# Performance work log

Measured on AMD Instinct MI355X. Metric: run time of the kernel, lower is better.

Reference implementation:

```python
import jax, jax.numpy as jnp
import numpy as np

B, D, NB, BS = 32, 2048, 16, 512  # batch, dim_input=dim_output, n_blocks, block_size; NB*BS*BS == D*D


def setup_inputs() -> dict:
    key = jax.random.key(0)
    k1, k2, k3, k4, k5 = jax.random.split(key, 5)
    x = jax.random.normal(k1, (B, D), dtype=jnp.float32)
    gate_w = jax.random.normal(k2, (D, NB), dtype=jnp.float32) / np.sqrt(D)
    gate_b = jax.random.normal(k3, (NB,), dtype=jnp.float32) * 0.02
    weight = jax.random.normal(k4, (D, D), dtype=jnp.float32) / np.sqrt(D)  # kaiming-uniform-like scale
    bias = jax.random.normal(k5, (D,), dtype=jnp.float32) * (1.0 / np.sqrt(D))
    return {"x": x, "gate_w": gate_w, "gate_b": gate_b, "weight": weight, "bias": bias}


def reference(x, gate_w, gate_b, weight, bias):
    b = x.shape[0]
    k_drop = NB // 2
    # gate network: Linear -> Sigmoid
    g = jax.nn.sigmoid(x @ gate_w + gate_b)  # (b, NB)
    # zero out the k smallest gates per sample (topk largest=False, scatter 0)
    _, drop_idx = jax.lax.top_k(-g, k_drop)  # indices of smallest gates
    rows = jnp.arange(b)[:, None]
    g = g.at[rows, drop_idx].set(0.0)
    # broadcast gates over block-diagonal chunks of weight
    w0 = weight.reshape(NB, BS, BS)
    gw = (g[:, :, None, None] * w0).reshape(b, D, D)  # (b, dim_output, dim_input)
    # batched matvec + bias
    return jnp.einsum('bij,bj->bi', gw, x) + bias
```

## Files before the change

### kernel.cpp

```cpp
#include <hip/hip_runtime.h>
#include <hip/hip_bf16.h>


#define D_DIM 2048
#define B_DIM 32
#define NB_DIM 16
#define NWAVE 8
#define KCHUNK (D_DIM / NWAVE)
#define PM_PAD 20

typedef __attribute__((ext_vector_type(4))) float f32x4;
typedef __attribute__((ext_vector_type(8))) float f32x8;
typedef __attribute__((ext_vector_type(8))) __bf16 bf16x8;

static __device__ __forceinline__ __bf16 f2bf(float f) {
    unsigned u = __builtin_bit_cast(unsigned, f);
    u += 0x7fffu + ((u >> 16) & 1u);
    unsigned short h = (unsigned short)(u >> 16);
    return __builtin_bit_cast(__bf16, h);
}

static __device__ __forceinline__ bf16x8 load_cvt8(const float* p) {
    const f32x8 v = *(const f32x8*)p;
    bf16x8 r;
#pragma unroll
    for (int i = 0; i < 8; ++i) r[i] = f2bf(v[i]);
    return r;
}

__global__ __launch_bounds__(256) void prep_kernel(
    const float* __restrict__ X,
    const float* __restrict__ GW,
    const float* __restrict__ GB,
    float* __restrict__ gates,
    __bf16* __restrict__ Xbf)
{
    __shared__ float red[NB_DIM][256];
    __shared__ float sg[NB_DIM];
    const int b = blockIdx.x;
    const int t = threadIdx.x;

    {
        const int idx = b * D_DIM + t * 8;
        *(bf16x8*)(Xbf + idx) = load_cvt8(X + idx);
    }

    float acc[NB_DIM];
#pragma unroll
    for (int n = 0; n < NB_DIM; ++n) acc[n] = 0.f;

#pragma unroll
    for (int i = 0; i < D_DIM / 256; ++i) {
        const int c = t + i * 256;
        const float xv = X[b * D_DIM + c];
        const float* gw = GW + c * NB_DIM;
#pragma unroll
        for (int n = 0; n < NB_DIM; ++n) acc[n] += xv * gw[n];
    }
#pragma unroll
    for (int n = 0; n < NB_DIM; ++n) red[n][t] = acc[n];
    __syncthreads();
    for (int s = 128; s > 0; s >>= 1) {
        if (t < s) {
#pragma unroll
            for (int n = 0; n < NB_DIM; ++n) red[n][t] += red[n][t + s];
        }
        __syncthreads();
    }
    if (t < NB_DIM) {
        const float v = red[t][0] + GB[t];
        sg[t] = 1.f / (1.f + __expf(-v));
    }
    __syncthreads();
    if (t < NB_DIM) {
        const float g = sg[t];
        int rank = 0;
#pragma unroll
        for (int m = 0; m < NB_DIM; ++m) {
            const float gm = sg[m];
            if (gm < g || (gm == g && m < t)) rank++;
        }
        gates[b * NB_DIM + t] = (rank >= NB_DIM / 2) ? g : 0.f;
    }
}

__global__ __launch_bounds__(512) void main_fused(
    const float* __restrict__ W,
    const __bf16* __restrict__ Xbf,
    const float* __restrict__ gates,
    const float* __restrict__ bias,
    float* __restrict__ out)
{
    __shared__ float pm[NWAVE * B_DIM * PM_PAD];

    const int rt   = blockIdx.x;
    const int wave = threadIdx.x >> 6;
    const int lane = threadIdx.x & 63;
    const int l15  = lane & 15;
    const int q    = lane >> 4;

    const int r0 = rt * 16;
    const int k0 = wave * KCHUNK;

    const float*  arow = W   + (size_t)(r0 + l15) * D_DIM + k0 + q * 8;
    const __bf16* b0p  = Xbf + (size_t)(l15)      * D_DIM + k0 + q * 8;
    const __bf16* b1p  = Xbf + (size_t)(l15 + 16) * D_DIM + k0 + q * 8;

    f32x4 acc0 = {0.f, 0.f, 0.f, 0.f};
    f32x4 acc1 = {0.f, 0.f, 0.f, 0.f};

#pragma unroll
    for (int kk = 0; kk < KCHUNK / 32; ++kk) {
        const bf16x8 av  = load_cvt8(arow + kk * 32);
        const bf16x8 bv0 = *(const bf16x8*)(b0p + kk * 32);
        const bf16x8 bv1 = *(const bf16x8*)(b1p + kk * 32);
        acc0 = __builtin_amdgcn_mfma_f32_16x16x32_bf16(av, bv0, acc0, 0, 0, 0);
        acc1 = __builtin_amdgcn_mfma_f32_16x16x32_bf16(av, bv1, acc1, 0, 0, 0);
    }

    float* base = pm + wave * (B_DIM * PM_PAD);
    *(f32x4*)(base + l15 * PM_PAD + q * 4)        = acc0;
    *(f32x4*)(base + (l15 + 16) * PM_PAD + q * 4) = acc1;
    __syncthreads();

    const int t   = threadIdx.x;
    const int lb  = t >> 4;
    const int row = t & 15;
    float s = 0.f;
#pragma unroll
    for (int w = 0; w < NWAVE; ++w)
        s += pm[w * (B_DIM * PM_PAD) + lb * PM_PAD + row];

    const float g  = gates[lb * NB_DIM + (r0 >> 7)];
    const float bi = bias[r0 + row];
    out[(size_t)lb * D_DIM + r0 + row] = g * s + bi;
}

extern "C" void kernel_launch(void* const* d_in, const int* in_sizes, int n_in,
                              void* d_out, int out_size, void* d_ws, size_t ws_size,
                              hipStream_t stream) {
    const float* x    = (const float*)d_in[0];
    const float* gw   = (const float*)d_in[1];
    const float* gb   = (const float*)d_in[2];
    const float* w    = (const float*)d_in[3];
    const float* bias = (const float*)d_in[4];
    float* out = (float*)d_out;

    float*  gates = (float*)d_ws;
    __bf16* Xbf   = (__bf16*)((char*)d_ws + 4096);

    prep_kernel<<<B_DIM, 256, 0, stream>>>(x, gw, gb, gates, Xbf);
    main_fused<<<D_DIM / 16, 512, 0, stream>>>(w, Xbf, gates, bias, out);
}
```

Measured before the change: 83.88 us.

## Split gate matvec across more blocks and fuse gate finalize into main GEMM

```diff
diff --git a/kernel.cpp b/kernel.cpp
--- a/kernel.cpp
+++ b/kernel.cpp
@@ -7,7 +7,6 @@
 #define NB_DIM 16
 #define NWAVE 8
 #define KCHUNK (D_DIM / NWAVE)
-#define PM_PAD 20
 
 typedef __attribute__((ext_vector_type(4))) float f32x4;
 typedef __attribute__((ext_vector_type(8))) float f32x8;
@@ -28,38 +27,33 @@
     return r;
 }
 
-__global__ __launch_bounds__(256) void prep_kernel(
+__global__ __launch_bounds__(256) void gate_part(
     const float* __restrict__ X,
     const float* __restrict__ GW,
-    const float* __restrict__ GB,
-    float* __restrict__ gates,
-    __bf16* __restrict__ Xbf)
+    float* __restrict__ gp)
 {
     __shared__ float red[NB_DIM][256];
-    __shared__ float sg[NB_DIM];
-    const int b = blockIdx.x;
-    const int t = threadIdx.x;
+    const int b  = blockIdx.x >> 3;
+    const int ks = blockIdx.x & 7;
+    const int t  = threadIdx.x;
+    const int c  = ks * 256 + t;
 
-    {
-        const int idx = b * D_DIM + t * 8;
-        *(bf16x8*)(Xbf + idx) = load_cvt8(X + idx);
-    }
-
-    float acc[NB_DIM];
-#pragma unroll
-    for (int n = 0; n < NB_DIM; ++n) acc[n] = 0.f;
+    const float xv = X[b * D_DIM + c];
+    const f32x4 g0 = *(const f32x4*)(GW + c * NB_DIM + 0);
+    const f32x4 g1 = *(const f32x4*)(GW + c * NB_DIM + 4);
+    const f32x4 g2 = *(const f32x4*)(GW + c * NB_DIM + 8);
+    const f32x4 g3 = *(const f32x4*)(GW + c * NB_DIM + 12);
 
 #pragma unroll
-    for (int i = 0; i < D_DIM / 256; ++i) {
-        const int c = t + i * 256;
-        const float xv = X[b * D_DIM + c];
-        const float* gw = GW + c * NB_DIM;
+    for (int n = 0; n < 4; ++n) red[n][t]      = xv * g0[n];
 #pragma unroll
-        for (int n = 0; n < NB_DIM; ++n) acc[n] += xv * gw[n];
-    }
+    for (int n = 0; n < 4; ++n) red[n + 4][t]  = xv * g1[n];
 #pragma unroll
-    for (int n = 0; n < NB_DIM; ++n) red[n][t] = acc[n];
+    for (int n = 0; n < 4; ++n) red[n + 8][t]  = xv * g2[n];
+#pragma unroll
+    for (int n = 0; n < 4; ++n) red[n + 12][t] = xv * g3[n];
     __syncthreads();
+
     for (int s = 128; s > 0; s >>= 1) {
         if (t < s) {
 #pragma unroll
@@ -67,33 +61,23 @@
         }
         __syncthreads();
     }
-    if (t < NB_DIM) {
-        const float v = red[t][0] + GB[t];
-        sg[t] = 1.f / (1.f + __expf(-v));
-    }
-    __syncthreads();
-    if (t < NB_DIM) {
-        const float g = sg[t];
-        int rank = 0;
-#pragma unroll
-        for (int m = 0; m < NB_DIM; ++m) {
-            const float gm = sg[m];
-            if (gm < g || (gm == g && m < t)) rank++;
-        }
-        gates[b * NB_DIM + t] = (rank >= NB_DIM / 2) ? g : 0.f;
-    }
+    if (t < NB_DIM) gp[b * (8 * NB_DIM) + ks * NB_DIM + t] = red[t][0];
 }
 
-__global__ __launch_bounds__(512) void main_fused(
+__global__ __launch_bounds__(512) void mega(
     const float* __restrict__ W,
-    const __bf16* __restrict__ Xbf,
-    const float* __restrict__ gates,
+    const float* __restrict__ X,
+    const float* __restrict__ gp,
+    const float* __restrict__ GB,
     const float* __restrict__ bias,
     float* __restrict__ out)
 {
-    __shared__ float pm[NWAVE * B_DIM * PM_PAD];
+    __shared__ float pm[NWAVE][16][20];
+    __shared__ float sg[16];
 
-    const int rt   = blockIdx.x;
+    const int bid  = blockIdx.x;
+    const int rt   = bid & 127;
+    const int bh   = bid >> 7;
     const int wave = threadIdx.x >> 6;
     const int lane = threadIdx.x & 63;
     const int l15  = lane & 15;
@@ -102,38 +86,57 @@
     const int r0 = rt * 16;
     const int k0 = wave * KCHUNK;
 
-    const float*  arow = W   + (size_t)(r0 + l15) * D_DIM + k0 + q * 8;
-    const __bf16* b0p  = Xbf + (size_t)(l15)      * D_DIM + k0 + q * 8;
-    const __bf16* b1p  = Xbf + (size_t)(l15 + 16) * D_DIM + k0 + q * 8;
+    const float* arow = W + (size_t)(r0 + l15) * D_DIM + k0 + q * 8;
+    const float* xrow = X + (size_t)(bh * 16 + l15) * D_DIM + k0 + q * 8;
 
-    f32x4 acc0 = {0.f, 0.f, 0.f, 0.f};
-    f32x4 acc1 = {0.f, 0.f, 0.f, 0.f};
-
+    f32x4 acc = {0.f, 0.f, 0.f, 0.f};
 #pragma unroll
     for (int kk = 0; kk < KCHUNK / 32; ++kk) {
-        const bf16x8 av  = load_cvt8(arow + kk * 32);
-        const bf16x8 bv0 = *(const bf16x8*)(b0p + kk * 32);
-        const bf16x8 bv1 = *(const bf16x8*)(b1p + kk * 32);
-        acc0 = __builtin_amdgcn_mfma_f32_16x16x32_bf16(av, bv0, acc0, 0, 0, 0);
-        acc1 = __builtin_amdgcn_mfma_f32_16x16x32_bf16(av, bv1, acc1, 0, 0, 0);
+        const bf16x8 av = load_cvt8(arow + kk * 32);
+        const bf16x8 bv = load_cvt8(xrow + kk * 32);
+        acc = __builtin_amdgcn_mfma_f32_16x16x32_bf16(av, bv, acc, 0, 0, 0);
     }
+    *(f32x4*)&pm[wave][l15][q * 4] = acc;
 
-    float* base = pm + wave * (B_DIM * PM_PAD);
-    *(f32x4*)(base + l15 * PM_PAD + q * 4)        = acc0;
-    *(f32x4*)(base + (l15 + 16) * PM_PAD + q * 4) = acc1;
+    if (threadIdx.x < NB_DIM) {
+        const int b = bh * 16 + threadIdx.x;
+        const float* p = gp + b * (8 * NB_DIM);
+        float lg[NB_DIM];
+#pragma unroll
+        for (int n = 0; n < NB_DIM; ++n) lg[n] = GB[n];
+#pragma unroll
+        for (int ks = 0; ks < 8; ++ks)
+#pragma unroll
+            for (int n = 0; n < NB_DIM; ++n) lg[n] += p[ks * NB_DIM + n];
+        float g[NB_DIM];
+#pragma unroll
+        for (int n = 0; n < NB_DIM; ++n) g[n] = 1.f / (1.f + __expf(-lg[n]));
+        const int nb = rt >> 3;
+        float gn = 0.f;
+#pragma unroll
+        for (int n = 0; n < NB_DIM; ++n) gn = (n == nb) ? g[n] : gn;
+        int rank = 0;
+#pragma unroll
+        for (int m = 0; m < NB_DIM; ++m)
+            if (g[m] < gn || (g[m] == gn && m < nb)) rank++;
+        sg[threadIdx.x] = (rank >= NB_DIM / 2) ? gn : 0.f;
+    }
     __syncthreads();
 
-    const int t   = threadIdx.x;
-    const int lb  = t >> 4;
-    const int row = t & 15;
-    float s = 0.f;
+    if (threadIdx.x < 64) {
+        const int lb = threadIdx.x >> 2;
+        const int r4 = (threadIdx.x & 3) * 4;
+        f32x4 s = {0.f, 0.f, 0.f, 0.f};
 #pragma unroll
-    for (int w = 0; w < NWAVE; ++w)
-        s += pm[w * (B_DIM * PM_PAD) + lb * PM_PAD + row];
-
-    const float g  = gates[lb * NB_DIM + (r0 >> 7)];
-    const float bi = bias[r0 + row];
-    out[(size_t)lb * D_DIM + r0 + row] = g * s + bi;
+        for (int w = 0; w < NWAVE; ++w)
+            s += *(const f32x4*)&pm[w][lb][r4];
+        const float gv = sg[lb];
+        const f32x4 bi = *(const f32x4*)(bias + r0 + r4);
+        f32x4 y;
+#pragma unroll
+        for (int i = 0; i < 4; ++i) y[i] = gv * s[i] + bi[i];
+        *(f32x4*)(out + (size_t)(bh * 16 + lb) * D_DIM + r0 + r4) = y;
+    }
 }
 
 extern "C" void kernel_launch(void* const* d_in, const int* in_sizes, int n_in,
@@ -146,9 +149,8 @@
     const float* bias = (const float*)d_in[4];
     float* out = (float*)d_out;
 
-    float*  gates = (float*)d_ws;
-    __bf16* Xbf   = (__bf16*)((char*)d_ws + 4096);
+    float* gp = (float*)d_ws;
 
-    prep_kernel<<<B_DIM, 256, 0, stream>>>(x, gw, gb, gates, Xbf);
-    main_fused<<<D_DIM / 16, 512, 0, stream>>>(w, Xbf, gates, bias, out);
+    gate_part<<<B_DIM * 8, 256, 0, stream>>>(x, gw, gp);
+    mega<<<256, 512, 0, stream>>>(w, x, gp, gb, bias, out);
 }
```

After: 83.05 us. About the same (-1.0%).
